# Kernel optimization log

Measured on AMD Instinct MI355X. Metric: run time of the kernel, lower is better.

Reference implementation:

```python
import jax, jax.numpy as jnp
import numpy as np

T, H, I, E, K = 4096, 1024, 2048, 32, 4


def setup_inputs() -> dict:
    key = jax.random.key(0)
    ks = jax.random.split(key, 8)
    s = lambda k, shape, std: (jax.random.normal(k, shape, jnp.float32) * std)
    return {
        "x": s(ks[0], (T, H), 1.0),
        "router_w": s(ks[1], (E, H), 0.02),
        "gate_w": s(ks[2], (E, H, I), 0.02),
        "up_w": s(ks[3], (E, H, I), 0.02),
        "down_w": s(ks[4], (E, I, H), 0.02),
        "shared_gate_w": s(ks[5], (H, I), 0.02),
        "shared_up_w": s(ks[6], (H, I), 0.02),
        "shared_down_w": s(ks[7], (I, H), 0.02),
        "top_k": K,
    }


def _moe_forward(x, router_w, gate_w, up_w, down_w, sg, su, sd, top_k):
    # x: [T, H]; expert weights: gate/up [E, H, I], down [E, I, H]
    Tn = x.shape[0]
    En = router_w.shape[0]

    # Router: softmax over experts, top-k selection, renormalize selected probs
    logits = x @ router_w.T                                   # [T, E]
    probs = jax.nn.softmax(logits, axis=-1)
    topk_p, topk_i = jax.lax.top_k(probs, top_k)              # [T, K]
    topk_p = topk_p / jnp.sum(topk_p, axis=-1, keepdims=True)

    # Dense combine weights: combine[t, e] = routing weight of expert e for token t
    combine = jnp.zeros((Tn, En), x.dtype).at[
        jnp.arange(Tn)[:, None], topk_i].add(topk_p)          # [T, E]

    def expert_step(acc, inp):
        wg, wu, wd, c = inp                                   # [H,I], [H,I], [I,H], [T]
        h = jax.nn.silu(x @ wg) * (x @ wu)                    # [T, I] SwiGLU
        return acc + c[:, None] * (h @ wd), None

    acc0 = jnp.zeros_like(x)
    out, _ = jax.lax.scan(expert_step, acc0,
                          (gate_w, up_w, down_w, combine.T))

    # Shared expert: always applied
    shared = (jax.nn.silu(x @ sg) * (x @ su)) @ sd            # [T, H]
    return out + shared


def reference(x, router_w, gate_w, up_w, down_w,
              shared_gate_w, shared_up_w, shared_down_w, top_k):
    return _moe_forward(x, router_w, gate_w, up_w, down_w,
                        shared_gate_w, shared_up_w, shared_down_w, top_k)
```

## Files before the change

kernel.cpp:

```cpp
#include <hip/hip_runtime.h>
#include <hip/hip_bf16.h>

#define T_TOK 4096
#define H_DIM 1024
#define I_DIM 2048
#define N_EXP 32
#define TOPK  4
#define TKTOT (T_TOK * TOPK)
#define ROWS_MAX 24576
#define MAX_TILES 192
#define BM 128
#define BK 64
#define LDB 72

typedef _Float16 f16;
typedef __attribute__((ext_vector_type(2))) f16  f16x2;
typedef __attribute__((ext_vector_type(4))) f16  f16x4;
typedef __attribute__((ext_vector_type(8))) f16  f16x8;
typedef __attribute__((ext_vector_type(4))) float f32x4;

__device__ __forceinline__ void glds16(const f16* g, f16* l) {
  __builtin_amdgcn_global_load_lds(
      (const __attribute__((address_space(1))) void*)g,
      (__attribute__((address_space(3))) void*)l, 16, 0, 0);
}
__device__ __forceinline__ void sfence() { __builtin_amdgcn_sched_barrier(0); }
__device__ __forceinline__ void bar_pre() {
  sfence();
  asm volatile("s_waitcnt lgkmcnt(0)" ::: "memory");
  sfence();
  __builtin_amdgcn_s_barrier();
  sfence();
}
__device__ __forceinline__ void bar_post() {
  sfence();
  __builtin_amdgcn_s_barrier();
  sfence();
}

__global__ void prep_kernel(const float* __restrict__ x, f16* __restrict__ xb,
                            int* __restrict__ row_token,
                            int* __restrict__ counts) {
  int gid = blockIdx.x * blockDim.x + threadIdx.x;
  float4 v = *(const float4*)(x + (size_t)gid * 4);
  f16x4 hv = { (f16)v.x, (f16)v.y, (f16)v.z, (f16)v.w };
  *(f16x4*)(xb + (size_t)gid * 4) = hv;
  if (gid < ROWS_MAX) row_token[gid] = (gid < T_TOK) ? gid : 0;
  if (gid < N_EXP) counts[gid] = 0;
}

__global__ void router_kernel(const float* __restrict__ x,
                              const float* __restrict__ rw,
                              int* __restrict__ expert_sel,
                              float* __restrict__ weight_sel,
                              int* __restrict__ counts) {
  int wid = threadIdx.x >> 6, lane = threadIdx.x & 63;
  int t = blockIdx.x * 4 + wid;
  float xr[16];
#pragma unroll
  for (int j = 0; j < 16; ++j) xr[j] = x[(size_t)t * H_DIM + lane + j * 64];
  float l[32];
#pragma unroll
  for (int e = 0; e < 32; ++e) {
    float p = 0.f;
#pragma unroll
    for (int j = 0; j < 16; ++j) p += xr[j] * rw[(size_t)e * H_DIM + lane + j * 64];
#pragma unroll
    for (int off = 32; off; off >>= 1) p += __shfl_xor(p, off, 64);
    l[e] = p;
  }
  if (lane == 0) {
    unsigned used = 0;
    int sel[4]; float lv[4];
#pragma unroll
    for (int k = 0; k < 4; ++k) {
      float bv = -3.4e38f; int bi = 0;
#pragma unroll
      for (int e = 0; e < 32; ++e) {
        bool better = (((used >> e) & 1u) == 0u) && (l[e] > bv);
        bv = better ? l[e] : bv;
        bi = better ? e : bi;
      }
      used |= 1u << bi; sel[k] = bi; lv[k] = bv;
    }
    float m = lv[0];
    float p0 = __expf(lv[0] - m), p1 = __expf(lv[1] - m);
    float p2 = __expf(lv[2] - m), p3 = __expf(lv[3] - m);
    float s = p0 + p1 + p2 + p3;
    float wv[4] = { p0 / s, p1 / s, p2 / s, p3 / s };
#pragma unroll
    for (int k = 0; k < 4; ++k) {
      expert_sel[t * 4 + k] = sel[k];
      weight_sel[t * 4 + k] = wv[k];
      atomicAdd(&counts[sel[k]], 1);
    }
  }
}

__global__ void scan_kernel(const int* __restrict__ counts, int* __restrict__ cursor,
                            int* __restrict__ tile_expert, int* __restrict__ tile_row0,
                            int* __restrict__ ntiles) {
  if (threadIdx.x != 0 || blockIdx.x != 0) return;
  int nt = 0;
  for (int i = 0; i < T_TOK / BM; ++i) { tile_expert[nt] = N_EXP; tile_row0[nt] = i * BM; ++nt; }
  int pos = T_TOK;
  for (int e = 0; e < N_EXP; ++e) {
    cursor[e] = pos;
    int c = counts[e];
    int nte = (c + BM - 1) / BM;
    for (int i = 0; i < nte; ++i) { tile_expert[nt] = e; tile_row0[nt] = pos + i * BM; ++nt; }
    pos += nte * BM;
  }
  ntiles[0] = nt;
}

__global__ void scatter_kernel(const int* __restrict__ expert_sel,
                               int* __restrict__ cursor,
                               int* __restrict__ row_token,
                               int* __restrict__ slot_of) {
  int i = blockIdx.x * blockDim.x + threadIdx.x;
  if (i >= TKTOT) return;
  int e = expert_sel[i];
  int pos = atomicAdd(&cursor[e], 1);
  row_token[pos] = i >> 2;
  slot_of[i] = pos;
}

struct Bf2 { float2 g[8]; };
__device__ __forceinline__ Bf2 fetch_b2(const float* __restrict__ src, size_t ldn) {
  Bf2 r;
#pragma unroll
  for (int j = 0; j < 8; ++j) r.g[j] = *(const float2*)(src + (size_t)j * ldn);
  return r;
}
__device__ __forceinline__ void write_b2(const Bf2& b,
                                         f16 (*__restrict__ Bs)[LDB], int nq, int kr) {
  const float* ga = (const float*)b.g;
  int ks = (8 * kr) ^ ((nq & 7) << 3);
#pragma unroll
  for (int i = 0; i < 2; ++i) {
    union { f16x2 p[4]; f16x8 v; } u;
#pragma unroll
    for (int j = 0; j < 4; ++j)
      u.p[j] = __builtin_bit_cast(
          f16x2, __builtin_amdgcn_cvt_pkrtz(ga[(2 * j) * 2 + i],
                                            ga[(2 * j + 1) * 2 + i]));
    *(f16x8*)&Bs[2 * nq + i][ks] = u.v;
  }
}
__device__ __forceinline__ int rswz1(int row, int kf16) {
  return kf16 ^ (((row >> 1) & 7) << 3);
}

struct Bf4 { float4 g[8]; };
__device__ __forceinline__ Bf4 fetch_b4(const float* __restrict__ src, size_t ldn) {
  Bf4 r;
#pragma unroll
  for (int j = 0; j < 8; ++j) r.g[j] = *(const float4*)(src + (size_t)j * ldn);
  return r;
}
__device__ __forceinline__ void write_b4(const Bf4& b,
                                         f16 (*__restrict__ Bs)[LDB], int nq, int kr) {
  const float* ga = (const float*)b.g;
  int ks = (8 * kr) ^ ((nq & 7) << 3);
#pragma unroll
  for (int i = 0; i < 4; ++i) {
    union { f16x2 p[4]; f16x8 v; } u;
#pragma unroll
    for (int j = 0; j < 4; ++j)
      u.p[j] = __builtin_bit_cast(
          f16x2, __builtin_amdgcn_cvt_pkrtz(ga[(2 * j) * 4 + i],
                                            ga[(2 * j + 1) * 4 + i]));
    *(f16x8*)&Bs[4 * nq + i][ks] = u.v;
  }
}
__device__ __forceinline__ int rswz2(int row, int kf16) {
  return kf16 ^ (((row >> 2) & 7) << 3);
}

__global__ __launch_bounds__(256, 3) void gemm1_kernel(
    const f16* __restrict__ xb,
    const float* __restrict__ gate_w, const float* __restrict__ up_w,
    const float* __restrict__ sgw, const float* __restrict__ suw,
    const int* __restrict__ row_token,
    const int* __restrict__ tile_expert, const int* __restrict__ tile_row0,
    const int* __restrict__ ntiles, f16* __restrict__ hbuf) {
  int d = blockIdx.y * gridDim.x + blockIdx.x;
  int l = (d & 7) * 768 + (d >> 3);
  int bx = l % MAX_TILES;
  int n0 = (l / MAX_TILES) * 64;
  if (bx >= ntiles[0]) return;
  int e = tile_expert[bx];
  int row0 = tile_row0[bx];
  const float* wg = (e < N_EXP) ? gate_w + (size_t)e * H_DIM * I_DIM : sgw;
  const float* wu = (e < N_EXP) ? up_w   + (size_t)e * H_DIM * I_DIM : suw;

  __shared__ __align__(16) f16 smem[2 * BM * BK + 2 * 64 * LDB];
  f16* A0 = smem;
  f16* A1 = smem + BM * BK;
  f16 (*Bg)[LDB] = (f16(*)[LDB])(smem + 2 * BM * BK);
  f16 (*Bu)[LDB] = (f16(*)[LDB])(smem + 2 * BM * BK + 64 * LDB);
  f16 (*Ct)[LDB] = (f16(*)[LDB])smem;

  int tid = threadIdx.x;
  int lane = tid & 63, wid = tid >> 6;
  int wm = wid >> 1, wn = wid & 1;
  int lr = lane & 15, lk = (lane >> 4) * 8;
  int nq = tid & 31, kr = tid >> 5;

  const f16* abase[4];
#pragma unroll
  for (int it = 0; it < 4; ++it) {
    int idx = tid + it * 256;
    int arow = idx >> 3;
    int atok = row_token[row0 + arow];
    abase[it] = xb + (size_t)atok * H_DIM + ((((idx & 7)) ^ (arow & 7)) << 3);
  }
  const float* wgp = wg + (size_t)(8 * kr) * I_DIM + n0 + 2 * nq;
  const float* wup = wu + (size_t)(8 * kr) * I_DIM + n0 + 2 * nq;

  f32x4 accg[4][2], accu[4][2];
#pragma unroll
  for (int m = 0; m < 4; ++m)
#pragma unroll
    for (int n = 0; n < 2; ++n) { accg[m][n] = (f32x4)0.f; accu[m][n] = (f32x4)0.f; }

  sfence();
#pragma unroll
  for (int it = 0; it < 4; ++it)
    glds16(abase[it], A0 + (tid + it * 256) * 8);
  sfence();
  Bf2 pg = fetch_b2(wgp, I_DIM);
  Bf2 pu = fetch_b2(wup, I_DIM);
  sfence();

  const int NK = H_DIM / BK;
  for (int ks = 0; ks < NK; ++ks) {
    write_b2(pg, Bg, nq, kr);
    write_b2(pu, Bu, nq, kr);
    if (ks + 1 < NK) {
      int k0n = (ks + 1) * BK;
      f16* ad = ((ks + 1) & 1) ? A1 : A0;
      sfence();
#pragma unroll
      for (int it = 0; it < 4; ++it)
        glds16(abase[it] + k0n, ad + (tid + it * 256) * 8);
      sfence();
      pg = fetch_b2(wgp + (size_t)k0n * I_DIM, I_DIM);
      pu = fetch_b2(wup + (size_t)k0n * I_DIM, I_DIM);
      sfence();
    }
    bar_pre();
    const f16* As = (ks & 1) ? A1 : A0;
    __builtin_amdgcn_s_setprio(1);
#pragma unroll
    for (int kk = 0; kk < BK; kk += 32) {
      f16x8 a[4], bg[2], bu[2];
#pragma unroll
      for (int m = 0; m < 4; ++m) {
        int ar = wm * 64 + m * 16 + lr;
        int ko = (kk + lk) ^ ((ar & 7) << 3);
        a[m] = *(const f16x8*)(As + ar * BK + ko);
      }
#pragma unroll
      for (int n = 0; n < 2; ++n) {
        int rowb = wn * 32 + n * 16 + lr;
        int ko = rswz1(rowb, kk + lk);
        bg[n] = *(const f16x8*)&Bg[rowb][ko];
        bu[n] = *(const f16x8*)&Bu[rowb][ko];
      }
#pragma unroll
      for (int m = 0; m < 4; ++m)
#pragma unroll
        for (int n = 0; n < 2; ++n) {
          accg[m][n] = __builtin_amdgcn_mfma_f32_16x16x32_f16(a[m], bg[n], accg[m][n], 0, 0, 0);
          accu[m][n] = __builtin_amdgcn_mfma_f32_16x16x32_f16(a[m], bu[n], accu[m][n], 0, 0, 0);
        }
    }
    __builtin_amdgcn_s_setprio(0);
    bar_post();
  }
#pragma unroll
  for (int m = 0; m < 4; ++m)
#pragma unroll
    for (int n = 0; n < 2; ++n)
#pragma unroll
      for (int j = 0; j < 4; ++j) {
        float g = accg[m][n][j], u = accu[m][n][j];
        float hv = g / (1.f + __expf(-g)) * u;
        Ct[wm * 64 + m * 16 + (lane >> 4) * 4 + j][wn * 32 + n * 16 + lr] = (f16)hv;
      }
  __syncthreads();
#pragma unroll
  for (int it = 0; it < 4; ++it) {
    int idx = tid + it * 256;
    int r = idx >> 3, g8 = (idx & 7) * 8;
    *(f16x8*)(hbuf + (size_t)(row0 + r) * I_DIM + n0 + g8) = *(const f16x8*)&Ct[r][g8];
  }
}

__global__ __launch_bounds__(256, 3) void gemm2_kernel(
    const f16* __restrict__ hbuf,
    const float* __restrict__ down_w, const float* __restrict__ sdw,
    const int* __restrict__ tile_expert, const int* __restrict__ tile_row0,
    const int* __restrict__ ntiles, f16* __restrict__ ybuf) {
  int d = blockIdx.y * gridDim.x + blockIdx.x;
  int l = (d & 7) * 192 + (d >> 3);
  int bx = l % MAX_TILES;
  int n0 = (l / MAX_TILES) * 128;
  if (bx >= ntiles[0]) return;
  int e = tile_expert[bx];
  int row0 = tile_row0[bx];
  const float* wd = (e < N_EXP) ? down_w + (size_t)e * I_DIM * H_DIM : sdw;

  __shared__ __align__(16) f16 smem[2 * BM * BK + 128 * LDB];
  f16* A0 = smem;
  f16* A1 = smem + BM * BK;
  f16 (*Bd)[LDB] = (f16(*)[LDB])(smem + 2 * BM * BK);
  f16 (*Ct)[136] = (f16(*)[136])smem;

  int tid = threadIdx.x;
  int lane = tid & 63, wid = tid >> 6;
  int wm = wid >> 1, wn = wid & 1;
  int lr = lane & 15, lk = (lane >> 4) * 8;
  int nq = tid & 31, kr = tid >> 5;

  const f16* abase[4];
#pragma unroll
  for (int it = 0; it < 4; ++it) {
    int idx = tid + it * 256;
    int arow = idx >> 3;
    abase[it] = hbuf + (size_t)(row0 + arow) * I_DIM + ((((idx & 7)) ^ (arow & 7)) << 3);
  }
  const float* wdp = wd + (size_t)(8 * kr) * H_DIM + n0 + 4 * nq;

  f32x4 acc[4][4];
#pragma unroll
  for (int m = 0; m < 4; ++m)
#pragma unroll
    for (int n = 0; n < 4; ++n) acc[m][n] = (f32x4)0.f;

  sfence();
#pragma unroll
  for (int it = 0; it < 4; ++it)
    glds16(abase[it], A0 + (tid + it * 256) * 8);
  sfence();
  Bf4 pd = fetch_b4(wdp, H_DIM);
  sfence();

  const int NK = I_DIM / BK;
  for (int ks = 0; ks < NK; ++ks) {
    write_b4(pd, Bd, nq, kr);
    if (ks + 1 < NK) {
      int k0n = (ks + 1) * BK;
      f16* ad = ((ks + 1) & 1) ? A1 : A0;
      sfence();
#pragma unroll
      for (int it = 0; it < 4; ++it)
        glds16(abase[it] + k0n, ad + (tid + it * 256) * 8);
      sfence();
      pd = fetch_b4(wdp + (size_t)k0n * H_DIM, H_DIM);
      sfence();
    }
    bar_pre();
    const f16* As = (ks & 1) ? A1 : A0;
    __builtin_amdgcn_s_setprio(1);
#pragma unroll
    for (int kk = 0; kk < BK; kk += 32) {
      f16x8 a[4], bd[4];
#pragma unroll
      for (int m = 0; m < 4; ++m) {
        int ar = wm * 64 + m * 16 + lr;
        int ko = (kk + lk) ^ ((ar & 7) << 3);
        a[m] = *(const f16x8*)(As + ar * BK + ko);
      }
#pragma unroll
      for (int n = 0; n < 4; ++n) {
        int rowb = wn * 64 + n * 16 + lr;
        bd[n] = *(const f16x8*)&Bd[rowb][rswz2(rowb, kk + lk)];
      }
#pragma unroll
      for (int m = 0; m < 4; ++m)
#pragma unroll
        for (int n = 0; n < 4; ++n)
          acc[m][n] = __builtin_amdgcn_mfma_f32_16x16x32_f16(a[m], bd[n], acc[m][n], 0, 0, 0);
    }
    __builtin_amdgcn_s_setprio(0);
    bar_post();
  }
#pragma unroll
  for (int m = 0; m < 4; ++m)
#pragma unroll
    for (int n = 0; n < 4; ++n)
#pragma unroll
      for (int j = 0; j < 4; ++j)
        Ct[wm * 64 + m * 16 + (lane >> 4) * 4 + j][wn * 64 + n * 16 + lr] =
            (f16)acc[m][n][j];
  __syncthreads();
#pragma unroll
  for (int it = 0; it < 8; ++it) {
    int idx = tid + it * 256;
    int r = idx >> 4, g8 = (idx & 15) * 8;
    *(f16x8*)(ybuf + (size_t)(row0 + r) * H_DIM + n0 + g8) = *(const f16x8*)&Ct[r][g8];
  }
}

__global__ void gather_kernel(const f16* __restrict__ ybuf,
                              const int* __restrict__ slot_of,
                              const float* __restrict__ weight_sel,
                              float* __restrict__ out) {
  int gid = blockIdx.x * blockDim.x + threadIdx.x;
  int t = gid >> 7, s8 = (gid & 127) * 8;
  f16x8 ysh = *(const f16x8*)(ybuf + (size_t)t * H_DIM + s8);
  float a[8];
#pragma unroll
  for (int j = 0; j < 8; ++j) a[j] = (float)ysh[j];
#pragma unroll
  for (int k = 0; k < 4; ++k) {
    int sl = slot_of[t * 4 + k];
    float w = weight_sel[t * 4 + k];
    f16x8 v = *(const f16x8*)(ybuf + (size_t)sl * H_DIM + s8);
#pragma unroll
    for (int j = 0; j < 8; ++j) a[j] += w * (float)v[j];
  }
  float4 o0 = { a[0], a[1], a[2], a[3] };
  float4 o1 = { a[4], a[5], a[6], a[7] };
  *(float4*)(out + (size_t)t * H_DIM + s8) = o0;
  *(float4*)(out + (size_t)t * H_DIM + s8 + 4) = o1;
}

extern "C" void kernel_launch(void* const* d_in, const int* in_sizes, int n_in,
                              void* d_out, int out_size, void* d_ws, size_t ws_size,
                              hipStream_t stream) {
  const float* x        = (const float*)d_in[0];
  const float* router_w = (const float*)d_in[1];
  const float* gate_w   = (const float*)d_in[2];
  const float* up_w     = (const float*)d_in[3];
  const float* down_w   = (const float*)d_in[4];
  const float* sgw      = (const float*)d_in[5];
  const float* suw      = (const float*)d_in[6];
  const float* sdw      = (const float*)d_in[7];
  float* out = (float*)d_out;

  char* w = (char*)d_ws;
  f16*   xb         = (f16*)w;   w += (size_t)T_TOK * H_DIM * 2;
  int*   expert_sel = (int*)w;   w += (size_t)TKTOT * 4;
  float* weight_sel = (float*)w; w += (size_t)TKTOT * 4;
  int*   slot_of    = (int*)w;   w += (size_t)TKTOT * 4;
  int*   counts     = (int*)w;   w += 256;
  int*   cursor     = (int*)w;   w += 256;
  int*   tile_exp   = (int*)w;   w += MAX_TILES * 4;
  int*   tile_row0  = (int*)w;   w += MAX_TILES * 4;
  int*   ntiles     = (int*)w;   w += 256;
  int*   row_token  = (int*)w;   w += (size_t)ROWS_MAX * 4;
  f16*   hbuf       = (f16*)w;   w += (size_t)ROWS_MAX * I_DIM * 2;
  f16*   ybuf       = (f16*)w;   w += (size_t)ROWS_MAX * H_DIM * 2;
  if ((size_t)(w - (char*)d_ws) > ws_size) return;

  prep_kernel<<<(T_TOK * H_DIM / 4) / 256, 256, 0, stream>>>(x, xb, row_token, counts);
  router_kernel<<<T_TOK / 4, 256, 0, stream>>>(x, router_w, expert_sel, weight_sel, counts);
  scan_kernel<<<1, 64, 0, stream>>>(counts, cursor, tile_exp, tile_row0, ntiles);
  scatter_kernel<<<TKTOT / 256, 256, 0, stream>>>(expert_sel, cursor, row_token, slot_of);
  gemm1_kernel<<<dim3(MAX_TILES, I_DIM / 64), 256, 0, stream>>>(
      xb, gate_w, up_w, sgw, suw, row_token, tile_exp, tile_row0, ntiles, hbuf);
  gemm2_kernel<<<dim3(MAX_TILES, H_DIM / 128), 256, 0, stream>>>(
      hbuf, down_w, sdw, tile_exp, tile_row0, ntiles, ybuf);
  gather_kernel<<<(T_TOK * (H_DIM / 8)) / 256, 256, 0, stream>>>(
      ybuf, slot_of, weight_sel, out);
}
```

Before: 653.0 us.

## Halve K tile, double-buffer B in LDS, drop second barrier, raise occupancy

Both expert GEMM kernels now use a K-step of 32 instead of 64. The B tile is double-buffered in LDS, which allows the trailing per-iteration barrier to be removed, leaving one barrier per K step. The LDS swizzles are redone for the narrower tile, and the launch bounds rise from 3 to 4 waves per SIMD to improve latency hiding. The cost is twice as many loop iterations and barriers, with less MFMA work between each sync, plus higher register pressure from the new bound.

```diff
diff --git a/kernel.cpp b/kernel.cpp
--- a/kernel.cpp
+++ b/kernel.cpp
@@ -10,8 +10,8 @@
 #define ROWS_MAX 24576
 #define MAX_TILES 192
 #define BM 128
-#define BK 64
-#define LDB 72
+#define BK 32
+#define LDB 40
 
 typedef _Float16 f16;
 typedef __attribute__((ext_vector_type(2))) f16  f16x2;
@@ -28,11 +28,6 @@
 __device__ __forceinline__ void bar_pre() {
   sfence();
   asm volatile("s_waitcnt lgkmcnt(0)" ::: "memory");
-  sfence();
-  __builtin_amdgcn_s_barrier();
-  sfence();
-}
-__device__ __forceinline__ void bar_post() {
   sfence();
   __builtin_amdgcn_s_barrier();
   sfence();
@@ -126,59 +121,35 @@
   slot_of[i] = pos;
 }
 
-struct Bf2 { float2 g[8]; };
-__device__ __forceinline__ Bf2 fetch_b2(const float* __restrict__ src, size_t ldn) {
-  Bf2 r;
+struct Bp { float2 g[8]; };
+__device__ __forceinline__ Bp fetch_bp(const float* __restrict__ src, size_t ldn) {
+  Bp r;
 #pragma unroll
   for (int j = 0; j < 8; ++j) r.g[j] = *(const float2*)(src + (size_t)j * ldn);
   return r;
 }
-__device__ __forceinline__ void write_b2(const Bf2& b,
-                                         f16 (*__restrict__ Bs)[LDB], int nq, int kr) {
+__device__ __forceinline__ void write_bp(const Bp& b, f16* __restrict__ Bs,
+                                         int c0, int kr) {
   const float* ga = (const float*)b.g;
-  int ks = (8 * kr) ^ ((nq & 7) << 3);
 #pragma unroll
   for (int i = 0; i < 2; ++i) {
     union { f16x2 p[4]; f16x8 v; } u;
 #pragma unroll
     for (int j = 0; j < 4; ++j)
       u.p[j] = __builtin_bit_cast(
-          f16x2, __builtin_amdgcn_cvt_pkrtz(ga[(2 * j) * 2 + i],
-                                            ga[(2 * j + 1) * 2 + i]));
-    *(f16x8*)&Bs[2 * nq + i][ks] = u.v;
-  }
-}
-__device__ __forceinline__ int rswz1(int row, int kf16) {
-  return kf16 ^ (((row >> 1) & 7) << 3);
-}
-
-struct Bf4 { float4 g[8]; };
-__device__ __forceinline__ Bf4 fetch_b4(const float* __restrict__ src, size_t ldn) {
-  Bf4 r;
-#pragma unroll
-  for (int j = 0; j < 8; ++j) r.g[j] = *(const float4*)(src + (size_t)j * ldn);
-  return r;
-}
-__device__ __forceinline__ void write_b4(const Bf4& b,
-                                         f16 (*__restrict__ Bs)[LDB], int nq, int kr) {
-  const float* ga = (const float*)b.g;
-  int ks = (8 * kr) ^ ((nq & 7) << 3);
-#pragma unroll
-  for (int i = 0; i < 4; ++i) {
-    union { f16x2 p[4]; f16x8 v; } u;
-#pragma unroll
-    for (int j = 0; j < 4; ++j)
-      u.p[j] = __builtin_bit_cast(
-          f16x2, __builtin_amdgcn_cvt_pkrtz(ga[(2 * j) * 4 + i],
-                                            ga[(2 * j + 1) * 4 + i]));
-    *(f16x8*)&Bs[4 * nq + i][ks] = u.v;
-  }
-}
-__device__ __forceinline__ int rswz2(int row, int kf16) {
-  return kf16 ^ (((row >> 2) & 7) << 3);
-}
-
-__global__ __launch_bounds__(256, 3) void gemm1_kernel(
+          f16x2, __builtin_amdgcn_cvt_pkrtz(ga[4 * j + i], ga[4 * j + 2 + i]));
+    int c = c0 + i;
+    *(f16x8*)(Bs + c * LDB + ((kr ^ ((c >> 3) & 3)) << 3)) = u.v;
+  }
+}
+__device__ __forceinline__ f16x8 bread(const f16* Bs, int row, int slot) {
+  return *(const f16x8*)(Bs + row * LDB + ((slot ^ ((row >> 3) & 3)) << 3));
+}
+__device__ __forceinline__ f16x8 aread(const f16* A, int row, int slot) {
+  return *(const f16x8*)(A + row * BK + ((slot ^ ((row >> 1) & 3)) << 3));
+}
+
+__global__ __launch_bounds__(256, 4) void gemm1_kernel(
     const f16* __restrict__ xb,
     const float* __restrict__ gate_w, const float* __restrict__ up_w,
     const float* __restrict__ sgw, const float* __restrict__ suw,
@@ -195,29 +166,33 @@
   const float* wg = (e < N_EXP) ? gate_w + (size_t)e * H_DIM * I_DIM : sgw;
   const float* wu = (e < N_EXP) ? up_w   + (size_t)e * H_DIM * I_DIM : suw;
 
-  __shared__ __align__(16) f16 smem[2 * BM * BK + 2 * 64 * LDB];
+  __shared__ __align__(16) f16 smem[2 * BM * BK + 2 * 2 * 64 * LDB];
   f16* A0 = smem;
   f16* A1 = smem + BM * BK;
-  f16 (*Bg)[LDB] = (f16(*)[LDB])(smem + 2 * BM * BK);
-  f16 (*Bu)[LDB] = (f16(*)[LDB])(smem + 2 * BM * BK + 64 * LDB);
-  f16 (*Ct)[LDB] = (f16(*)[LDB])smem;
+  f16* Bbase = smem + 2 * BM * BK;
+  f16 (*Ct)[72] = (f16(*)[72])smem;
 
   int tid = threadIdx.x;
-  int lane = tid & 63, wid = tid >> 6;
+  int lane = tid & 63;
+  int wid = tid >> 6;
   int wm = wid >> 1, wn = wid & 1;
-  int lr = lane & 15, lk = (lane >> 4) * 8;
-  int nq = tid & 31, kr = tid >> 5;
-
-  const f16* abase[4];
-#pragma unroll
-  for (int it = 0; it < 4; ++it) {
+  int lr = lane & 15, slot = lane >> 4;
+
+  int mat = tid >> 7;
+  int t7 = tid & 127;
+  int c0 = 2 * (t7 & 31);
+  int kr = t7 >> 5;
+  const float* wsrc = (mat ? wu : wg) + (size_t)(kr * 8) * I_DIM + n0 + c0;
+
+  const f16* abase[2];
+#pragma unroll
+  for (int it = 0; it < 2; ++it) {
     int idx = tid + it * 256;
-    int arow = idx >> 3;
+    int arow = idx >> 2;
+    int sl = idx & 3;
     int atok = row_token[row0 + arow];
-    abase[it] = xb + (size_t)atok * H_DIM + ((((idx & 7)) ^ (arow & 7)) << 3);
-  }
-  const float* wgp = wg + (size_t)(8 * kr) * I_DIM + n0 + 2 * nq;
-  const float* wup = wu + (size_t)(8 * kr) * I_DIM + n0 + 2 * nq;
+    abase[it] = xb + (size_t)atok * H_DIM + ((sl ^ ((arow >> 1) & 3)) << 3);
+  }
 
   f32x4 accg[4][2], accu[4][2];
 #pragma unroll
@@ -227,59 +202,53 @@
 
   sfence();
 #pragma unroll
-  for (int it = 0; it < 4; ++it)
+  for (int it = 0; it < 2; ++it)
     glds16(abase[it], A0 + (tid + it * 256) * 8);
   sfence();
-  Bf2 pg = fetch_b2(wgp, I_DIM);
-  Bf2 pu = fetch_b2(wup, I_DIM);
+  Bp pb = fetch_bp(wsrc, I_DIM);
   sfence();
 
   const int NK = H_DIM / BK;
   for (int ks = 0; ks < NK; ++ks) {
-    write_b2(pg, Bg, nq, kr);
-    write_b2(pu, Bu, nq, kr);
+    int buf = ks & 1;
+    f16* Bmat = Bbase + buf * 5120 + mat * 2560;
+    write_bp(pb, Bmat, c0, kr);
     if (ks + 1 < NK) {
       int k0n = (ks + 1) * BK;
-      f16* ad = ((ks + 1) & 1) ? A1 : A0;
-      sfence();
-#pragma unroll
-      for (int it = 0; it < 4; ++it)
+      f16* ad = buf ? A0 : A1;
+      sfence();
+#pragma unroll
+      for (int it = 0; it < 2; ++it)
         glds16(abase[it] + k0n, ad + (tid + it * 256) * 8);
       sfence();
-      pg = fetch_b2(wgp + (size_t)k0n * I_DIM, I_DIM);
-      pu = fetch_b2(wup + (size_t)k0n * I_DIM, I_DIM);
+      pb = fetch_bp(wsrc + (size_t)k0n * I_DIM, I_DIM);
       sfence();
     }
     bar_pre();
-    const f16* As = (ks & 1) ? A1 : A0;
+    const f16* As = buf ? A1 : A0;
+    const f16* Bg = Bbase + buf * 5120;
+    const f16* Bu = Bg + 2560;
     __builtin_amdgcn_s_setprio(1);
-#pragma unroll
-    for (int kk = 0; kk < BK; kk += 32) {
-      f16x8 a[4], bg[2], bu[2];
-#pragma unroll
-      for (int m = 0; m < 4; ++m) {
-        int ar = wm * 64 + m * 16 + lr;
-        int ko = (kk + lk) ^ ((ar & 7) << 3);
-        a[m] = *(const f16x8*)(As + ar * BK + ko);
+    f16x8 a[4], bg[2], bu[2];
+#pragma unroll
+    for (int m = 0; m < 4; ++m)
+      a[m] = aread(As, wm * 64 + m * 16 + lr, slot);
+#pragma unroll
+    for (int n = 0; n < 2; ++n) {
+      int rowb = wn * 32 + n * 16 + lr;
+      bg[n] = bread(Bg, rowb, slot);
+      bu[n] = bread(Bu, rowb, slot);
+    }
+#pragma unroll
+    for (int m = 0; m < 4; ++m)
+#pragma unroll
+      for (int n = 0; n < 2; ++n) {
+        accg[m][n] = __builtin_amdgcn_mfma_f32_16x16x32_f16(a[m], bg[n], accg[m][n], 0, 0, 0);
+        accu[m][n] = __builtin_amdgcn_mfma_f32_16x16x32_f16(a[m], bu[n], accu[m][n], 0, 0, 0);
       }
-#pragma unroll
-      for (int n = 0; n < 2; ++n) {
-        int rowb = wn * 32 + n * 16 + lr;
-        int ko = rswz1(rowb, kk + lk);
-        bg[n] = *(const f16x8*)&Bg[rowb][ko];
-        bu[n] = *(const f16x8*)&Bu[rowb][ko];
-      }
-#pragma unroll
-      for (int m = 0; m < 4; ++m)
-#pragma unroll
-        for (int n = 0; n < 2; ++n) {
-          accg[m][n] = __builtin_amdgcn_mfma_f32_16x16x32_f16(a[m], bg[n], accg[m][n], 0, 0, 0);
-          accu[m][n] = __builtin_amdgcn_mfma_f32_16x16x32_f16(a[m], bu[n], accu[m][n], 0, 0, 0);
-        }
-    }
     __builtin_amdgcn_s_setprio(0);
-    bar_post();
-  }
+  }
+  __syncthreads();
 #pragma unroll
   for (int m = 0; m < 4; ++m)
 #pragma unroll
@@ -288,7 +257,7 @@
       for (int j = 0; j < 4; ++j) {
         float g = accg[m][n][j], u = accu[m][n][j];
         float hv = g / (1.f + __expf(-g)) * u;
-        Ct[wm * 64 + m * 16 + (lane >> 4) * 4 + j][wn * 32 + n * 16 + lr] = (f16)hv;
+        Ct[wm * 64 + m * 16 + slot * 4 + j][wn * 32 + n * 16 + lr] = (f16)hv;
       }
   __syncthreads();
 #pragma unroll
@@ -299,7 +268,7 @@
   }
 }
 
-__global__ __launch_bounds__(256, 3) void gemm2_kernel(
+__global__ __launch_bounds__(256, 4) void gemm2_kernel(
     const f16* __restrict__ hbuf,
     const float* __restrict__ down_w, const float* __restrict__ sdw,
     const int* __restrict__ tile_expert, const int* __restrict__ tile_row0,
@@ -313,26 +282,30 @@
   int row0 = tile_row0[bx];
   const float* wd = (e < N_EXP) ? down_w + (size_t)e * I_DIM * H_DIM : sdw;
 
-  __shared__ __align__(16) f16 smem[2 * BM * BK + 128 * LDB];
+  __shared__ __align__(16) f16 smem[2 * BM * BK + 2 * 128 * LDB];
   f16* A0 = smem;
   f16* A1 = smem + BM * BK;
-  f16 (*Bd)[LDB] = (f16(*)[LDB])(smem + 2 * BM * BK);
+  f16* Bbase = smem + 2 * BM * BK;
   f16 (*Ct)[136] = (f16(*)[136])smem;
 
   int tid = threadIdx.x;
-  int lane = tid & 63, wid = tid >> 6;
+  int lane = tid & 63;
+  int wid = tid >> 6;
   int wm = wid >> 1, wn = wid & 1;
-  int lr = lane & 15, lk = (lane >> 4) * 8;
-  int nq = tid & 31, kr = tid >> 5;
-
-  const f16* abase[4];
-#pragma unroll
-  for (int it = 0; it < 4; ++it) {
+  int lr = lane & 15, slot = lane >> 4;
+
+  int c0 = 2 * (tid & 63);
+  int kr = tid >> 6;
+  const float* wsrc = wd + (size_t)(kr * 8) * H_DIM + n0 + c0;
+
+  const f16* abase[2];
+#pragma unroll
+  for (int it = 0; it < 2; ++it) {
     int idx = tid + it * 256;
-    int arow = idx >> 3;
-    abase[it] = hbuf + (size_t)(row0 + arow) * I_DIM + ((((idx & 7)) ^ (arow & 7)) << 3);
-  }
-  const float* wdp = wd + (size_t)(8 * kr) * H_DIM + n0 + 4 * nq;
+    int arow = idx >> 2;
+    int sl = idx & 3;
+    abase[it] = hbuf + (size_t)(row0 + arow) * I_DIM + ((sl ^ ((arow >> 1) & 3)) << 3);
+  }
 
   f32x4 acc[4][4];
 #pragma unroll
@@ -342,59 +315,53 @@
 
   sfence();
 #pragma unroll
-  for (int it = 0; it < 4; ++it)
+  for (int it = 0; it < 2; ++it)
     glds16(abase[it], A0 + (tid + it * 256) * 8);
   sfence();
-  Bf4 pd = fetch_b4(wdp, H_DIM);
+  Bp pb = fetch_bp(wsrc, H_DIM);
   sfence();
 
   const int NK = I_DIM / BK;
   for (int ks = 0; ks < NK; ++ks) {
-    write_b4(pd, Bd, nq, kr);
+    int buf = ks & 1;
+    write_bp(pb, Bbase + buf * 5120, c0, kr);
     if (ks + 1 < NK) {
       int k0n = (ks + 1) * BK;
-      f16* ad = ((ks + 1) & 1) ? A1 : A0;
-      sfence();
-#pragma unroll
-      for (int it = 0; it < 4; ++it)
+      f16* ad = buf ? A0 : A1;
+      sfence();
+#pragma unroll
+      for (int it = 0; it < 2; ++it)
         glds16(abase[it] + k0n, ad + (tid + it * 256) * 8);
       sfence();
-      pd = fetch_b4(wdp + (size_t)k0n * H_DIM, H_DIM);
+      pb = fetch_bp(wsrc + (size_t)k0n * H_DIM, H_DIM);
       sfence();
     }
     bar_pre();
-    const f16* As = (ks & 1) ? A1 : A0;
+    const f16* As = buf ? A1 : A0;
+    const f16* Bd = Bbase + buf * 5120;
     __builtin_amdgcn_s_setprio(1);
-#pragma unroll
-    for (int kk = 0; kk < BK; kk += 32) {
-      f16x8 a[4], bd[4];
-#pragma unroll
-      for (int m = 0; m < 4; ++m) {
-        int ar = wm * 64 + m * 16 + lr;
-        int ko = (kk + lk) ^ ((ar & 7) << 3);
-        a[m] = *(const f16x8*)(As + ar * BK + ko);
-      }
-#pragma unroll
-      for (int n = 0; n < 4; ++n) {
-        int rowb = wn * 64 + n * 16 + lr;
-        bd[n] = *(const f16x8*)&Bd[rowb][rswz2(rowb, kk + lk)];
-      }
-#pragma unroll
-      for (int m = 0; m < 4; ++m)
-#pragma unroll
-        for (int n = 0; n < 4; ++n)
-          acc[m][n] = __builtin_amdgcn_mfma_f32_16x16x32_f16(a[m], bd[n], acc[m][n], 0, 0, 0);
-    }
+    f16x8 a[4], bd[4];
+#pragma unroll
+    for (int m = 0; m < 4; ++m)
+      a[m] = aread(As, wm * 64 + m * 16 + lr, slot);
+#pragma unroll
+    for (int n = 0; n < 4; ++n)
+      bd[n] = bread(Bd, wn * 64 + n * 16 + lr, slot);
+#pragma unroll
+    for (int m = 0; m < 4; ++m)
+#pragma unroll
+      for (int n = 0; n < 4; ++n)
+        acc[m][n] = __builtin_amdgcn_mfma_f32_16x16x32_f16(a[m], bd[n], acc[m][n], 0, 0, 0);
     __builtin_amdgcn_s_setprio(0);
-    bar_post();
-  }
+  }
+  __syncthreads();
 #pragma unroll
   for (int m = 0; m < 4; ++m)
 #pragma unroll
     for (int n = 0; n < 4; ++n)
 #pragma unroll
       for (int j = 0; j < 4; ++j)
-        Ct[wm * 64 + m * 16 + (lane >> 4) * 4 + j][wn * 64 + n * 16 + lr] =
+        Ct[wm * 64 + m * 16 + slot * 4 + j][wn * 64 + n * 16 + lr] =
             (f16)acc[m][n][j];
   __syncthreads();
 #pragma unroll
```

Result: slower. 722.7 us (+10.7%).

## Deepen weight prefetch to two stages with partial vmcnt waits in MoE GEMMs

Applied to the files above, without the earlier changes.

Both expert GEMM kernels now keep two register-staged weight tiles in flight and unroll the K loop by two. Barriers wait only for the older loads, using explicit vmcnt thresholds instead of draining all memory ops. The goal is to hide global weight-load latency behind MFMA work. This adds register pressure, relies on hand-counted vmcnt values being correct, and issues redundant clamped loads at the tail.

```diff
diff --git a/kernel.cpp b/kernel.cpp
--- a/kernel.cpp
+++ b/kernel.cpp
@@ -25,16 +25,28 @@
       (__attribute__((address_space(3))) void*)l, 16, 0, 0);
 }
 __device__ __forceinline__ void sfence() { __builtin_amdgcn_sched_barrier(0); }
-__device__ __forceinline__ void bar_pre() {
-  sfence();
-  asm volatile("s_waitcnt lgkmcnt(0)" ::: "memory");
+__device__ __forceinline__ void bar_vm36() {
+  sfence();
+  asm volatile("s_waitcnt vmcnt(36) lgkmcnt(0)" ::: "memory");
   sfence();
   __builtin_amdgcn_s_barrier();
   sfence();
 }
+__device__ __forceinline__ void bar_vm20() {
+  sfence();
+  asm volatile("s_waitcnt vmcnt(20) lgkmcnt(0)" ::: "memory");
+  sfence();
+  __builtin_amdgcn_s_barrier();
+  sfence();
+}
 __device__ __forceinline__ void bar_post() {
   sfence();
   __builtin_amdgcn_s_barrier();
+  sfence();
+}
+__device__ __forceinline__ void drain_vm() {
+  sfence();
+  asm volatile("s_waitcnt vmcnt(0)" ::: "memory");
   sfence();
 }
 
@@ -225,61 +237,91 @@
 #pragma unroll
     for (int n = 0; n < 2; ++n) { accg[m][n] = (f32x4)0.f; accu[m][n] = (f32x4)0.f; }
 
+  const int NK = H_DIM / BK;
+
   sfence();
 #pragma unroll
   for (int it = 0; it < 4; ++it)
     glds16(abase[it], A0 + (tid + it * 256) * 8);
   sfence();
-  Bf2 pg = fetch_b2(wgp, I_DIM);
-  Bf2 pu = fetch_b2(wup, I_DIM);
-  sfence();
-
-  const int NK = H_DIM / BK;
-  for (int ks = 0; ks < NK; ++ks) {
-    write_b2(pg, Bg, nq, kr);
-    write_b2(pu, Bu, nq, kr);
-    if (ks + 1 < NK) {
-      int k0n = (ks + 1) * BK;
-      f16* ad = ((ks + 1) & 1) ? A1 : A0;
+  Bf2 g0 = fetch_b2(wgp, I_DIM);
+  Bf2 u0 = fetch_b2(wup, I_DIM);
+  sfence();
+  Bf2 g1 = fetch_b2(wgp + (size_t)BK * I_DIM, I_DIM);
+  Bf2 u1 = fetch_b2(wup + (size_t)BK * I_DIM, I_DIM);
+  sfence();
+
+#define G1_MFMA(ASRC)                                                        \
+  {                                                                          \
+    const f16* As_ = (ASRC);                                                 \
+    __builtin_amdgcn_s_setprio(1);                                           \
+    _Pragma("unroll")                                                        \
+    for (int kk = 0; kk < BK; kk += 32) {                                    \
+      f16x8 a[4], bg[2], bu[2];                                              \
+      _Pragma("unroll")                                                      \
+      for (int m = 0; m < 4; ++m) {                                          \
+        int ar = wm * 64 + m * 16 + lr;                                      \
+        int ko = (kk + lk) ^ ((ar & 7) << 3);                                \
+        a[m] = *(const f16x8*)(As_ + ar * BK + ko);                          \
+      }                                                                      \
+      _Pragma("unroll")                                                      \
+      for (int n = 0; n < 2; ++n) {                                          \
+        int rowb = wn * 32 + n * 16 + lr;                                    \
+        int ko = rswz1(rowb, kk + lk);                                       \
+        bg[n] = *(const f16x8*)&Bg[rowb][ko];                                \
+        bu[n] = *(const f16x8*)&Bu[rowb][ko];                                \
+      }                                                                      \
+      _Pragma("unroll")                                                      \
+      for (int m = 0; m < 4; ++m)                                            \
+        _Pragma("unroll")                                                    \
+        for (int n = 0; n < 2; ++n) {                                        \
+          accg[m][n] = __builtin_amdgcn_mfma_f32_16x16x32_f16(a[m], bg[n], accg[m][n], 0, 0, 0); \
+          accu[m][n] = __builtin_amdgcn_mfma_f32_16x16x32_f16(a[m], bu[n], accu[m][n], 0, 0, 0); \
+        }                                                                    \
+    }                                                                        \
+    __builtin_amdgcn_s_setprio(0);                                           \
+  }
+
+  for (int ks = 0; ks < NK; ks += 2) {
+    {
+      write_b2(g0, Bg, nq, kr);
+      write_b2(u0, Bu, nq, kr);
+      int ka = ((ks + 1 < NK) ? ks + 1 : NK - 1) * BK;
       sfence();
 #pragma unroll
       for (int it = 0; it < 4; ++it)
-        glds16(abase[it] + k0n, ad + (tid + it * 256) * 8);
-      sfence();
-      pg = fetch_b2(wgp + (size_t)k0n * I_DIM, I_DIM);
-      pu = fetch_b2(wup + (size_t)k0n * I_DIM, I_DIM);
-      sfence();
+        glds16(abase[it] + ka, A1 + (tid + it * 256) * 8);
+      sfence();
+      int kb = ((ks + 2 < NK) ? ks + 2 : NK - 1) * BK;
+      g0 = fetch_b2(wgp + (size_t)kb * I_DIM, I_DIM);
+      u0 = fetch_b2(wup + (size_t)kb * I_DIM, I_DIM);
+      sfence();
+      bar_vm36();
+      G1_MFMA(A0);
+      bar_post();
     }
-    bar_pre();
-    const f16* As = (ks & 1) ? A1 : A0;
-    __builtin_amdgcn_s_setprio(1);
-#pragma unroll
-    for (int kk = 0; kk < BK; kk += 32) {
-      f16x8 a[4], bg[2], bu[2];
-#pragma unroll
-      for (int m = 0; m < 4; ++m) {
-        int ar = wm * 64 + m * 16 + lr;
-        int ko = (kk + lk) ^ ((ar & 7) << 3);
-        a[m] = *(const f16x8*)(As + ar * BK + ko);
-      }
-#pragma unroll
-      for (int n = 0; n < 2; ++n) {
-        int rowb = wn * 32 + n * 16 + lr;
-        int ko = rswz1(rowb, kk + lk);
-        bg[n] = *(const f16x8*)&Bg[rowb][ko];
-        bu[n] = *(const f16x8*)&Bu[rowb][ko];
-      }
-#pragma unroll
-      for (int m = 0; m < 4; ++m)
-#pragma unroll
-        for (int n = 0; n < 2; ++n) {
-          accg[m][n] = __builtin_amdgcn_mfma_f32_16x16x32_f16(a[m], bg[n], accg[m][n], 0, 0, 0);
-          accu[m][n] = __builtin_amdgcn_mfma_f32_16x16x32_f16(a[m], bu[n], accu[m][n], 0, 0, 0);
-        }
+    {
+      write_b2(g1, Bg, nq, kr);
+      write_b2(u1, Bu, nq, kr);
+      int ka = ((ks + 2 < NK) ? ks + 2 : NK - 1) * BK;
+      sfence();
+#pragma unroll
+      for (int it = 0; it < 4; ++it)
+        glds16(abase[it] + ka, A0 + (tid + it * 256) * 8);
+      sfence();
+      int kb = ((ks + 3 < NK) ? ks + 3 : NK - 1) * BK;
+      g1 = fetch_b2(wgp + (size_t)kb * I_DIM, I_DIM);
+      u1 = fetch_b2(wup + (size_t)kb * I_DIM, I_DIM);
+      sfence();
+      bar_vm36();
+      G1_MFMA(A1);
+      bar_post();
     }
-    __builtin_amdgcn_s_setprio(0);
-    bar_post();
-  }
+  }
+#undef G1_MFMA
+
+  drain_vm();
+  __syncthreads();
 #pragma unroll
   for (int m = 0; m < 4; ++m)
 #pragma unroll
@@ -340,54 +382,81 @@
 #pragma unroll
     for (int n = 0; n < 4; ++n) acc[m][n] = (f32x4)0.f;
 
+  const int NK = I_DIM / BK;
+
   sfence();
 #pragma unroll
   for (int it = 0; it < 4; ++it)
     glds16(abase[it], A0 + (tid + it * 256) * 8);
   sfence();
-  Bf4 pd = fetch_b4(wdp, H_DIM);
-  sfence();
-
-  const int NK = I_DIM / BK;
-  for (int ks = 0; ks < NK; ++ks) {
-    write_b4(pd, Bd, nq, kr);
-    if (ks + 1 < NK) {
-      int k0n = (ks + 1) * BK;
-      f16* ad = ((ks + 1) & 1) ? A1 : A0;
+  Bf4 d0 = fetch_b4(wdp, H_DIM);
+  sfence();
+  Bf4 d1 = fetch_b4(wdp + (size_t)BK * H_DIM, H_DIM);
+  sfence();
+
+#define G2_MFMA(ASRC)                                                        \
+  {                                                                          \
+    const f16* As_ = (ASRC);                                                 \
+    __builtin_amdgcn_s_setprio(1);                                           \
+    _Pragma("unroll")                                                        \
+    for (int kk = 0; kk < BK; kk += 32) {                                    \
+      f16x8 a[4], bd[4];                                                     \
+      _Pragma("unroll")                                                      \
+      for (int m = 0; m < 4; ++m) {                                          \
+        int ar = wm * 64 + m * 16 + lr;                                      \
+        int ko = (kk + lk) ^ ((ar & 7) << 3);                                \
+        a[m] = *(const f16x8*)(As_ + ar * BK + ko);                          \
+      }                                                                      \
+      _Pragma("unroll")                                                      \
+      for (int n = 0; n < 4; ++n) {                                          \
+        int rowb = wn * 64 + n * 16 + lr;                                    \
+        bd[n] = *(const f16x8*)&Bd[rowb][rswz2(rowb, kk + lk)];              \
+      }                                                                      \
+      _Pragma("unroll")                                                      \
+      for (int m = 0; m < 4; ++m)                                            \
+        _Pragma("unroll")                                                    \
+        for (int n = 0; n < 4; ++n)                                          \
+          acc[m][n] = __builtin_amdgcn_mfma_f32_16x16x32_f16(a[m], bd[n], acc[m][n], 0, 0, 0); \
+    }                                                                        \
+    __builtin_amdgcn_s_setprio(0);                                           \
+  }
+
+  for (int ks = 0; ks < NK; ks += 2) {
+    {
+      write_b4(d0, Bd, nq, kr);
+      int ka = ((ks + 1 < NK) ? ks + 1 : NK - 1) * BK;
       sfence();
 #pragma unroll
       for (int it = 0; it < 4; ++it)
-        glds16(abase[it] + k0n, ad + (tid + it * 256) * 8);
-      sfence();
-      pd = fetch_b4(wdp + (size_t)k0n * H_DIM, H_DIM);
-      sfence();
+        glds16(abase[it] + ka, A1 + (tid + it * 256) * 8);
+      sfence();
+      int kb = ((ks + 2 < NK) ? ks + 2 : NK - 1) * BK;
+      d0 = fetch_b4(wdp + (size_t)kb * H_DIM, H_DIM);
+      sfence();
+      bar_vm20();
+      G2_MFMA(A0);
+      bar_post();
     }
-    bar_pre();
-    const f16* As = (ks & 1) ? A1 : A0;
-    __builtin_amdgcn_s_setprio(1);
-#pragma unroll
-    for (int kk = 0; kk < BK; kk += 32) {
-      f16x8 a[4], bd[4];
-#pragma unroll
-      for (int m = 0; m < 4; ++m) {
-        int ar = wm * 64 + m * 16 + lr;
-        int ko = (kk + lk) ^ ((ar & 7) << 3);
-        a[m] = *(const f16x8*)(As + ar * BK + ko);
-      }
-#pragma unroll
-      for (int n = 0; n < 4; ++n) {
-        int rowb = wn * 64 + n * 16 + lr;
-        bd[n] = *(const f16x8*)&Bd[rowb][rswz2(rowb, kk + lk)];
-      }
-#pragma unroll
-      for (int m = 0; m < 4; ++m)
-#pragma unroll
-        for (int n = 0; n < 4; ++n)
-          acc[m][n] = __builtin_amdgcn_mfma_f32_16x16x32_f16(a[m], bd[n], acc[m][n], 0, 0, 0);
+    {
+      write_b4(d1, Bd, nq, kr);
+      int ka = ((ks + 2 < NK) ? ks + 2 : NK - 1) * BK;
+      sfence();
+#pragma unroll
+      for (int it = 0; it < 4; ++it)
+        glds16(abase[it] + ka, A0 + (tid + it * 256) * 8);
+      sfence();
+      int kb = ((ks + 3 < NK) ? ks + 3 : NK - 1) * BK;
+      d1 = fetch_b4(wdp + (size_t)kb * H_DIM, H_DIM);
+      sfence();
+      bar_vm20();
+      G2_MFMA(A1);
+      bar_post();
     }
-    __builtin_amdgcn_s_setprio(0);
-    bar_post();
-  }
+  }
+#undef G2_MFMA
+
+  drain_vm();
+  __syncthreads();
 #pragma unroll
   for (int m = 0; m < 4; ++m)
 #pragma unroll
```

Result: slower. 1.325 ms (+103.0%).

## Load A operands directly to registers and double-buffer B tiles with one barrier

Applied to the files above, without the earlier changes.

Both MoE GEMM kernels stop staging the activation (A) tile through LDS via global_load_lds and instead have each lane load its MFMA A fragments straight from global memory into registers. The LDS is now used to double-buffer the converted weight (B) tiles, which removes the second barrier per K step. The single-threaded scan kernel is replaced with a wave-level shuffle prefix sum. This trades LDS traffic and a barrier for uncached per-lane global reads of A, which are redundant across waves sharing rows and may expose more global latency.

```diff
diff --git a/kernel.cpp b/kernel.cpp
--- a/kernel.cpp
+++ b/kernel.cpp
@@ -19,20 +19,10 @@
 typedef __attribute__((ext_vector_type(8))) f16  f16x8;
 typedef __attribute__((ext_vector_type(4))) float f32x4;
 
-__device__ __forceinline__ void glds16(const f16* g, f16* l) {
-  __builtin_amdgcn_global_load_lds(
-      (const __attribute__((address_space(1))) void*)g,
-      (__attribute__((address_space(3))) void*)l, 16, 0, 0);
-}
 __device__ __forceinline__ void sfence() { __builtin_amdgcn_sched_barrier(0); }
 __device__ __forceinline__ void bar_pre() {
   sfence();
   asm volatile("s_waitcnt lgkmcnt(0)" ::: "memory");
-  sfence();
-  __builtin_amdgcn_s_barrier();
-  sfence();
-}
-__device__ __forceinline__ void bar_post() {
   sfence();
   __builtin_amdgcn_s_barrier();
   sfence();
@@ -100,18 +90,32 @@
 __global__ void scan_kernel(const int* __restrict__ counts, int* __restrict__ cursor,
                             int* __restrict__ tile_expert, int* __restrict__ tile_row0,
                             int* __restrict__ ntiles) {
-  if (threadIdx.x != 0 || blockIdx.x != 0) return;
-  int nt = 0;
-  for (int i = 0; i < T_TOK / BM; ++i) { tile_expert[nt] = N_EXP; tile_row0[nt] = i * BM; ++nt; }
-  int pos = T_TOK;
-  for (int e = 0; e < N_EXP; ++e) {
-    cursor[e] = pos;
-    int c = counts[e];
-    int nte = (c + BM - 1) / BM;
-    for (int i = 0; i < nte; ++i) { tile_expert[nt] = e; tile_row0[nt] = pos + i * BM; ++nt; }
-    pos += nte * BM;
-  }
-  ntiles[0] = nt;
+  int lane = threadIdx.x;
+  if (lane < T_TOK / BM) { tile_expert[lane] = N_EXP; tile_row0[lane] = lane * BM; }
+  int nte = 0, rows = 0;
+  if (lane < N_EXP) {
+    int c = counts[lane];
+    nte = (c + BM - 1) / BM;
+    rows = nte * BM;
+  }
+  int pnte = nte, prows = rows;
+#pragma unroll
+  for (int off = 1; off < 64; off <<= 1) {
+    int t1 = __shfl_up(pnte, off, 64);
+    int t2 = __shfl_up(prows, off, 64);
+    if (lane >= off) { pnte += t1; prows += t2; }
+  }
+  int excl_nte = pnte - nte, excl_rows = prows - rows;
+  if (lane < N_EXP) {
+    int pos = T_TOK + excl_rows;
+    cursor[lane] = pos;
+    int tb = T_TOK / BM + excl_nte;
+    for (int i = 0; i < nte; ++i) {
+      tile_expert[tb + i] = lane;
+      tile_row0[tb + i] = pos + i * BM;
+    }
+    if (lane == N_EXP - 1) ntiles[0] = tb + nte;
+  }
 }
 
 __global__ void scatter_kernel(const int* __restrict__ expert_sel,
@@ -133,8 +137,8 @@
   for (int j = 0; j < 8; ++j) r.g[j] = *(const float2*)(src + (size_t)j * ldn);
   return r;
 }
-__device__ __forceinline__ void write_b2(const Bf2& b,
-                                         f16 (*__restrict__ Bs)[LDB], int nq, int kr) {
+__device__ __forceinline__ void write_b2(const Bf2& b, f16* __restrict__ Bs,
+                                         int nq, int kr) {
   const float* ga = (const float*)b.g;
   int ks = (8 * kr) ^ ((nq & 7) << 3);
 #pragma unroll
@@ -145,7 +149,7 @@
       u.p[j] = __builtin_bit_cast(
           f16x2, __builtin_amdgcn_cvt_pkrtz(ga[(2 * j) * 2 + i],
                                             ga[(2 * j + 1) * 2 + i]));
-    *(f16x8*)&Bs[2 * nq + i][ks] = u.v;
+    *(f16x8*)(Bs + (2 * nq + i) * LDB + ks) = u.v;
   }
 }
 __device__ __forceinline__ int rswz1(int row, int kf16) {
@@ -159,8 +163,8 @@
   for (int j = 0; j < 8; ++j) r.g[j] = *(const float4*)(src + (size_t)j * ldn);
   return r;
 }
-__device__ __forceinline__ void write_b4(const Bf4& b,
-                                         f16 (*__restrict__ Bs)[LDB], int nq, int kr) {
+__device__ __forceinline__ void write_b4(const Bf4& b, f16* __restrict__ Bs,
+                                         int nq, int kr) {
   const float* ga = (const float*)b.g;
   int ks = (8 * kr) ^ ((nq & 7) << 3);
 #pragma unroll
@@ -171,7 +175,7 @@
       u.p[j] = __builtin_bit_cast(
           f16x2, __builtin_amdgcn_cvt_pkrtz(ga[(2 * j) * 4 + i],
                                             ga[(2 * j + 1) * 4 + i]));
-    *(f16x8*)&Bs[4 * nq + i][ks] = u.v;
+    *(f16x8*)(Bs + (4 * nq + i) * LDB + ks) = u.v;
   }
 }
 __device__ __forceinline__ int rswz2(int row, int kf16) {
@@ -195,11 +199,7 @@
   const float* wg = (e < N_EXP) ? gate_w + (size_t)e * H_DIM * I_DIM : sgw;
   const float* wu = (e < N_EXP) ? up_w   + (size_t)e * H_DIM * I_DIM : suw;
 
-  __shared__ __align__(16) f16 smem[2 * BM * BK + 2 * 64 * LDB];
-  f16* A0 = smem;
-  f16* A1 = smem + BM * BK;
-  f16 (*Bg)[LDB] = (f16(*)[LDB])(smem + 2 * BM * BK);
-  f16 (*Bu)[LDB] = (f16(*)[LDB])(smem + 2 * BM * BK + 64 * LDB);
+  __shared__ __align__(16) f16 smem[2 * 2 * 64 * LDB];
   f16 (*Ct)[LDB] = (f16(*)[LDB])smem;
 
   int tid = threadIdx.x;
@@ -210,11 +210,9 @@
 
   const f16* abase[4];
 #pragma unroll
-  for (int it = 0; it < 4; ++it) {
-    int idx = tid + it * 256;
-    int arow = idx >> 3;
-    int atok = row_token[row0 + arow];
-    abase[it] = xb + (size_t)atok * H_DIM + ((((idx & 7)) ^ (arow & 7)) << 3);
+  for (int m = 0; m < 4; ++m) {
+    int atok = row_token[row0 + wm * 64 + m * 16 + lr];
+    abase[m] = xb + (size_t)atok * H_DIM + lk;
   }
   const float* wgp = wg + (size_t)(8 * kr) * I_DIM + n0 + 2 * nq;
   const float* wup = wu + (size_t)(8 * kr) * I_DIM + n0 + 2 * nq;
@@ -225,61 +223,66 @@
 #pragma unroll
     for (int n = 0; n < 2; ++n) { accg[m][n] = (f32x4)0.f; accu[m][n] = (f32x4)0.f; }
 
-  sfence();
-#pragma unroll
-  for (int it = 0; it < 4; ++it)
-    glds16(abase[it], A0 + (tid + it * 256) * 8);
-  sfence();
+  const int NK = H_DIM / BK;
   Bf2 pg = fetch_b2(wgp, I_DIM);
   Bf2 pu = fetch_b2(wup, I_DIM);
   sfence();
 
-  const int NK = H_DIM / BK;
   for (int ks = 0; ks < NK; ++ks) {
-    write_b2(pg, Bg, nq, kr);
-    write_b2(pu, Bu, nq, kr);
+    f16* Bgw = smem + (ks & 1) * 9216;
+    f16* Buw = Bgw + 4608;
+    write_b2(pg, Bgw, nq, kr);
+    write_b2(pu, Buw, nq, kr);
     if (ks + 1 < NK) {
-      int k0n = (ks + 1) * BK;
-      f16* ad = ((ks + 1) & 1) ? A1 : A0;
-      sfence();
-#pragma unroll
-      for (int it = 0; it < 4; ++it)
-        glds16(abase[it] + k0n, ad + (tid + it * 256) * 8);
-      sfence();
-      pg = fetch_b2(wgp + (size_t)k0n * I_DIM, I_DIM);
-      pu = fetch_b2(wup + (size_t)k0n * I_DIM, I_DIM);
-      sfence();
-    }
+      pg = fetch_b2(wgp + (size_t)(ks + 1) * BK * I_DIM, I_DIM);
+      pu = fetch_b2(wup + (size_t)(ks + 1) * BK * I_DIM, I_DIM);
+    }
+    int k0 = ks * BK;
+    f16x8 a0[4];
+#pragma unroll
+    for (int m = 0; m < 4; ++m) a0[m] = *(const f16x8*)(abase[m] + k0);
     bar_pre();
-    const f16* As = (ks & 1) ? A1 : A0;
     __builtin_amdgcn_s_setprio(1);
-#pragma unroll
-    for (int kk = 0; kk < BK; kk += 32) {
-      f16x8 a[4], bg[2], bu[2];
-#pragma unroll
-      for (int m = 0; m < 4; ++m) {
-        int ar = wm * 64 + m * 16 + lr;
-        int ko = (kk + lk) ^ ((ar & 7) << 3);
-        a[m] = *(const f16x8*)(As + ar * BK + ko);
-      }
+    {
+      f16x8 bg[2], bu[2];
 #pragma unroll
       for (int n = 0; n < 2; ++n) {
         int rowb = wn * 32 + n * 16 + lr;
-        int ko = rswz1(rowb, kk + lk);
-        bg[n] = *(const f16x8*)&Bg[rowb][ko];
-        bu[n] = *(const f16x8*)&Bu[rowb][ko];
+        int ko = rswz1(rowb, lk);
+        bg[n] = *(const f16x8*)(Bgw + rowb * LDB + ko);
+        bu[n] = *(const f16x8*)(Buw + rowb * LDB + ko);
       }
 #pragma unroll
       for (int m = 0; m < 4; ++m)
 #pragma unroll
         for (int n = 0; n < 2; ++n) {
-          accg[m][n] = __builtin_amdgcn_mfma_f32_16x16x32_f16(a[m], bg[n], accg[m][n], 0, 0, 0);
-          accu[m][n] = __builtin_amdgcn_mfma_f32_16x16x32_f16(a[m], bu[n], accu[m][n], 0, 0, 0);
+          accg[m][n] = __builtin_amdgcn_mfma_f32_16x16x32_f16(a0[m], bg[n], accg[m][n], 0, 0, 0);
+          accu[m][n] = __builtin_amdgcn_mfma_f32_16x16x32_f16(a0[m], bu[n], accu[m][n], 0, 0, 0);
         }
     }
+    {
+      f16x8 a1[4], bg[2], bu[2];
+#pragma unroll
+      for (int m = 0; m < 4; ++m) a1[m] = *(const f16x8*)(abase[m] + k0 + 32);
+#pragma unroll
+      for (int n = 0; n < 2; ++n) {
+        int rowb = wn * 32 + n * 16 + lr;
+        int ko = rswz1(rowb, 32 + lk);
+        bg[n] = *(const f16x8*)(Bgw + rowb * LDB + ko);
+        bu[n] = *(const f16x8*)(Buw + rowb * LDB + ko);
+      }
+#pragma unroll
+      for (int m = 0; m < 4; ++m)
+#pragma unroll
+        for (int n = 0; n < 2; ++n) {
+          accg[m][n] = __builtin_amdgcn_mfma_f32_16x16x32_f16(a1[m], bg[n], accg[m][n], 0, 0, 0);
+          accu[m][n] = __builtin_amdgcn_mfma_f32_16x16x32_f16(a1[m], bu[n], accu[m][n], 0, 0, 0);
+        }
+    }
     __builtin_amdgcn_s_setprio(0);
-    bar_post();
-  }
+  }
+
+  __syncthreads();
 #pragma unroll
   for (int m = 0; m < 4; ++m)
 #pragma unroll
@@ -313,10 +316,7 @@
   int row0 = tile_row0[bx];
   const float* wd = (e < N_EXP) ? down_w + (size_t)e * I_DIM * H_DIM : sdw;
 
-  __shared__ __align__(16) f16 smem[2 * BM * BK + 128 * LDB];
-  f16* A0 = smem;
-  f16* A1 = smem + BM * BK;
-  f16 (*Bd)[LDB] = (f16(*)[LDB])(smem + 2 * BM * BK);
+  __shared__ __align__(16) f16 smem[2 * 128 * LDB];
   f16 (*Ct)[136] = (f16(*)[136])smem;
 
   int tid = threadIdx.x;
@@ -327,11 +327,8 @@
 
   const f16* abase[4];
 #pragma unroll
-  for (int it = 0; it < 4; ++it) {
-    int idx = tid + it * 256;
-    int arow = idx >> 3;
-    abase[it] = hbuf + (size_t)(row0 + arow) * I_DIM + ((((idx & 7)) ^ (arow & 7)) << 3);
-  }
+  for (int m = 0; m < 4; ++m)
+    abase[m] = hbuf + (size_t)(row0 + wm * 64 + m * 16 + lr) * I_DIM + lk;
   const float* wdp = wd + (size_t)(8 * kr) * H_DIM + n0 + 4 * nq;
 
   f32x4 acc[4][4];
@@ -340,54 +337,53 @@
 #pragma unroll
     for (int n = 0; n < 4; ++n) acc[m][n] = (f32x4)0.f;
 
-  sfence();
-#pragma unroll
-  for (int it = 0; it < 4; ++it)
-    glds16(abase[it], A0 + (tid + it * 256) * 8);
-  sfence();
+  const int NK = I_DIM / BK;
   Bf4 pd = fetch_b4(wdp, H_DIM);
   sfence();
 
-  const int NK = I_DIM / BK;
   for (int ks = 0; ks < NK; ++ks) {
-    write_b4(pd, Bd, nq, kr);
-    if (ks + 1 < NK) {
-      int k0n = (ks + 1) * BK;
-      f16* ad = ((ks + 1) & 1) ? A1 : A0;
-      sfence();
-#pragma unroll
-      for (int it = 0; it < 4; ++it)
-        glds16(abase[it] + k0n, ad + (tid + it * 256) * 8);
-      sfence();
-      pd = fetch_b4(wdp + (size_t)k0n * H_DIM, H_DIM);
-      sfence();
-    }
+    f16* Bdw = smem + (ks & 1) * 9216;
+    write_b4(pd, Bdw, nq, kr);
+    if (ks + 1 < NK)
+      pd = fetch_b4(wdp + (size_t)(ks + 1) * BK * H_DIM, H_DIM);
+    int k0 = ks * BK;
+    f16x8 a0[4];
+#pragma unroll
+    for (int m = 0; m < 4; ++m) a0[m] = *(const f16x8*)(abase[m] + k0);
     bar_pre();
-    const f16* As = (ks & 1) ? A1 : A0;
     __builtin_amdgcn_s_setprio(1);
-#pragma unroll
-    for (int kk = 0; kk < BK; kk += 32) {
-      f16x8 a[4], bd[4];
-#pragma unroll
-      for (int m = 0; m < 4; ++m) {
-        int ar = wm * 64 + m * 16 + lr;
-        int ko = (kk + lk) ^ ((ar & 7) << 3);
-        a[m] = *(const f16x8*)(As + ar * BK + ko);
-      }
+    {
+      f16x8 bd[4];
 #pragma unroll
       for (int n = 0; n < 4; ++n) {
         int rowb = wn * 64 + n * 16 + lr;
-        bd[n] = *(const f16x8*)&Bd[rowb][rswz2(rowb, kk + lk)];
+        bd[n] = *(const f16x8*)(Bdw + rowb * LDB + rswz2(rowb, lk));
       }
 #pragma unroll
       for (int m = 0; m < 4; ++m)
 #pragma unroll
         for (int n = 0; n < 4; ++n)
-          acc[m][n] = __builtin_amdgcn_mfma_f32_16x16x32_f16(a[m], bd[n], acc[m][n], 0, 0, 0);
+          acc[m][n] = __builtin_amdgcn_mfma_f32_16x16x32_f16(a0[m], bd[n], acc[m][n], 0, 0, 0);
+    }
+    {
+      f16x8 a1[4], bd[4];
+#pragma unroll
+      for (int m = 0; m < 4; ++m) a1[m] = *(const f16x8*)(abase[m] + k0 + 32);
+#pragma unroll
+      for (int n = 0; n < 4; ++n) {
+        int rowb = wn * 64 + n * 16 + lr;
+        bd[n] = *(const f16x8*)(Bdw + rowb * LDB + rswz2(rowb, 32 + lk));
+      }
+#pragma unroll
+      for (int m = 0; m < 4; ++m)
+#pragma unroll
+        for (int n = 0; n < 4; ++n)
+          acc[m][n] = __builtin_amdgcn_mfma_f32_16x16x32_f16(a1[m], bd[n], acc[m][n], 0, 0, 0);
     }
     __builtin_amdgcn_s_setprio(0);
-    bar_post();
-  }
+  }
+
+  __syncthreads();
 #pragma unroll
   for (int m = 0; m < 4; ++m)
 #pragma unroll
```

New measurement: 940.4 us. 44.0% more time.
